# Kernel optimization log

Measured on AMD Instinct MI355X. Metric: run time of the kernel, lower is better.

Reference implementation:

```python
import jax, jax.numpy as jnp
import numpy as np

N_USERS = 100000
N_ITEMS = 50000
N_NODES = N_USERS + N_ITEMS
EMB_DIM = 64
N_EDGES = 1200000
N_LAYERS = 3


def setup_inputs() -> dict:
    key = jax.random.key(0)
    k1, k2, k3, k4, k5 = jax.random.split(key, 5)
    edge_row = jax.random.randint(k1, (N_EDGES,), 0, N_NODES, dtype=jnp.int32)
    edge_col = jax.random.randint(k2, (N_EDGES,), 0, N_NODES, dtype=jnp.int32)
    edge_weight = jax.random.uniform(k3, (N_EDGES,), dtype=jnp.float32)
    # xavier_uniform for nn.Embedding: bound = sqrt(6/(fan_in+fan_out))
    bu = float(np.sqrt(6.0 / (N_USERS + EMB_DIM)))
    bi = float(np.sqrt(6.0 / (N_ITEMS + EMB_DIM)))
    user_emb = jax.random.uniform(k4, (N_USERS, EMB_DIM), jnp.float32, -bu, bu)
    item_emb = jax.random.uniform(k5, (N_ITEMS, EMB_DIM), jnp.float32, -bi, bi)
    return {
        "edge_row": edge_row,
        "edge_col": edge_col,
        "edge_weight": edge_weight,
        "user_emb": user_emb,
        "item_emb": item_emb,
    }


def _spmm(edge_row, edge_col, edge_weight, x):
    # y[i] = sum_{e: row[e]==i} w[e] * x[col[e]]  (COO sparse @ dense)
    gathered = x[edge_col] * edge_weight[:, None]  # [E, d]
    return jax.ops.segment_sum(gathered, edge_row, num_segments=N_NODES)


def reference(edge_row, edge_col, edge_weight, user_emb, item_emb):
    x = jnp.concatenate([user_emb, item_emb], axis=0)  # [N, d]
    acc = x  # running sum over layer outputs (layer 0 = initial embeddings)
    for _ in range(N_LAYERS):
        x = _spmm(edge_row, edge_col, edge_weight, x)
        acc = acc + x
    mean_emb = acc / (N_LAYERS + 1)
    return mean_emb[:N_USERS], mean_emb[N_USERS:]
```

## Files before the change

### kernel.cpp

```cpp
#include <hip/hip_runtime.h>
#include <hip/hip_bf16.h>


#define EMB 64
#define BUCKET_SHIFT 9
#define BROWS (1 << BUCKET_SHIFT)
#define NBUCK_PAD 320
#define S1_CHUNK 2048
#define BCAP 4608
#define S2_CAP 6
#define SPMM_BLOCKS 2048

typedef _Float16 h8 __attribute__((ext_vector_type(8)));
typedef _Float16 h2v __attribute__((ext_vector_type(2)));
typedef float f2v __attribute__((ext_vector_type(2)));
typedef float f4 __attribute__((ext_vector_type(4)));
typedef int i2v __attribute__((ext_vector_type(2)));

union H8U { h8 v; h2v p[4]; };

__global__ void s1_convert(const int* __restrict__ row, const int* __restrict__ col,
                           const float* __restrict__ w, int* __restrict__ cursor1,
                           int2* __restrict__ tmp,
                           const float* __restrict__ ue, const float* __restrict__ ie,
                           h8* __restrict__ X0h, int nu_elems, int total8,
                           int E, int s1Blocks) {
    int t = threadIdx.x;
    if ((int)blockIdx.x < s1Blocks) {
        __shared__ int lcount[NBUCK_PAD];
        __shared__ int lbase[NBUCK_PAD];
        int c0 = blockIdx.x * S1_CHUNK;
        if (t < NBUCK_PAD) lcount[t] = 0;
        __syncthreads();
        int pkc[S1_CHUNK / 512];
        int cc[S1_CHUNK / 512];
        int rr[S1_CHUNK / 512];
        float ww[S1_CHUNK / 512];
        #pragma unroll
        for (int i = 0; i < S1_CHUNK / 512; i++) {
            int e = c0 + i * 512 + t;
            pkc[i] = -1;
            if (e < E) {
                int r = row[e];
                int b = r >> BUCKET_SHIFT;
                int rank = atomicAdd(&lcount[b], 1);
                pkc[i] = (b << 12) | rank;
                cc[i] = col[e];
                rr[i] = r & (BROWS - 1);
                ww[i] = w[e];
            }
        }
        __syncthreads();
        if (t < NBUCK_PAD) {
            int c = lcount[t];
            if (c) lbase[t] = atomicAdd(&cursor1[t], c);
        }
        __syncthreads();
        #pragma unroll
        for (int i = 0; i < S1_CHUNK / 512; i++) {
            if (pkc[i] >= 0) {
                int b = pkc[i] >> 12;
                int pos = lbase[b] + (pkc[i] & 4095);
                if (pos < BCAP)
                    tmp[(size_t)b * BCAP + pos] =
                        make_int2((cc[i] << BUCKET_SHIFT) | rr[i], __float_as_int(ww[i]));
            }
        }
    } else {
        int g = (blockIdx.x - s1Blocks) * 512 + t;
        if (g >= total8) return;
        int base = g << 3;
        const f4* src = (const f4*)((base < nu_elems) ? (ue + base)
                                                      : (ie + (base - nu_elems)));
        f4 a = src[0], b = src[1];
        h8 o;
        o[0] = (_Float16)a.x; o[1] = (_Float16)a.y; o[2] = (_Float16)a.z; o[3] = (_Float16)a.w;
        o[4] = (_Float16)b.x; o[5] = (_Float16)b.y; o[6] = (_Float16)b.z; o[7] = (_Float16)b.w;
        X0h[g] = o;
    }
}

__global__ void scatter2(const int* __restrict__ cursor1, const int2* __restrict__ tmp,
                         int2* __restrict__ cw, int* __restrict__ rbeg,
                         int* __restrict__ rend, int nrows) {
    __shared__ int cnt[BROWS];
    __shared__ int wS[8];
    int t = threadIdx.x;
    int j = blockIdx.x;
    int rowbase = j << BUCKET_SHIFT;
    int rows_here = nrows - rowbase;
    if (rows_here > BROWS) rows_here = BROWS;
    int num = cursor1[j];
    if (num > BCAP) num = BCAP;
    int base = j * BCAP;
    int iters = (num + 1023) >> 10;

    if (t < BROWS) cnt[t] = 0;
    __syncthreads();

    int pkc[S2_CAP];
    int rk[S2_CAP];
    int wv[S2_CAP];
    bool cached = (iters <= S2_CAP);
    if (cached) {
        for (int i = 0; i < iters; i++) {
            int p = i * 1024 + t;
            pkc[i] = -1;
            if (p < num) {
                int2 rec = tmp[base + p];
                pkc[i] = rec.x;
                wv[i] = rec.y;
                rk[i] = atomicAdd(&cnt[rec.x & (BROWS - 1)], 1);
            }
        }
    } else {
        for (int p = t; p < num; p += 1024)
            atomicAdd(&cnt[tmp[base + p].x & (BROWS - 1)], 1);
    }
    __syncthreads();

    int lane = t & 63;
    int wave = t >> 6;
    int v = 0, s = 0;
    if (t < BROWS) {
        v = cnt[t];
        s = v;
        #pragma unroll
        for (int off = 1; off < 64; off <<= 1) {
            int tt = __shfl_up(s, off, 64);
            if (lane >= off) s += tt;
        }
        if (lane == 63) wS[wave] = s;
    }
    __syncthreads();
    if (t < BROWS) {
        int woff = 0;
        for (int w = 0; w < wave; w++) woff += wS[w];
        int excl = woff + s - v;
        if (t < rows_here) {
            rbeg[rowbase + t] = base + excl;
            rend[rowbase + t] = base + excl + v;
        }
        s = excl;
    }
    __syncthreads();
    if (t < BROWS) cnt[t] = s;
    __syncthreads();

    if (cached) {
        for (int i = 0; i < iters; i++) {
            if (pkc[i] >= 0) {
                int r = pkc[i] & (BROWS - 1);
                cw[base + cnt[r] + rk[i]] = make_int2(pkc[i] >> BUCKET_SHIFT, wv[i]);
            }
        }
    } else {
        for (int p = t; p < num; p += 1024) {
            int2 rec = tmp[base + p];
            int r = rec.x & (BROWS - 1);
            int pos = atomicAdd(&cnt[r], 1);
            cw[base + pos] = make_int2(rec.x >> BUCKET_SHIFT, rec.y);
        }
    }
}

template <bool LAST>
__global__ __launch_bounds__(256) void spmm_kernel(
        const int* __restrict__ rbeg, const int* __restrict__ rend,
        const i2v* __restrict__ cw,
        const h8* __restrict__ Xin, h8* __restrict__ Xout,
        const h8* __restrict__ X0, const h8* __restrict__ X1,
        float* __restrict__ out, int nrows) {
    int lane = threadIdx.x & 63;
    int g = lane >> 3;
    int l8 = lane & 7;
    int wv = (blockIdx.x * blockDim.x + threadIdx.x) >> 6;
    int totWaves = (gridDim.x * blockDim.x) >> 6;

    for (int base8 = wv * 8; base8 < nrows; base8 += totWaves * 8) {
        int row = base8 + g;
        bool valid = row < nrows;
        int beg = valid ? rbeg[row] : 0;
        int end = valid ? rend[row] : 0;

        f2v acc2[4];
        #pragma unroll
        for (int k = 0; k < 4; k++) acc2[k] = (f2v){0.f, 0.f};

        int e = beg;
        for (; e + 3 < end; e += 4) {
            i2v c0 = cw[e];
            i2v c1 = cw[e + 1];
            i2v c2 = cw[e + 2];
            i2v c3 = cw[e + 3];
            H8U v0, v1, v2, v3;
            v0.v = Xin[(c0.x << 3) + l8];
            v1.v = Xin[(c1.x << 3) + l8];
            v2.v = Xin[(c2.x << 3) + l8];
            v3.v = Xin[(c3.x << 3) + l8];
            f2v w0p = (f2v){__int_as_float(c0.y), __int_as_float(c0.y)};
            f2v w1p = (f2v){__int_as_float(c1.y), __int_as_float(c1.y)};
            f2v w2p = (f2v){__int_as_float(c2.y), __int_as_float(c2.y)};
            f2v w3p = (f2v){__int_as_float(c3.y), __int_as_float(c3.y)};
            #pragma unroll
            for (int k = 0; k < 4; k++) {
                acc2[k] += w0p * __builtin_convertvector(v0.p[k], f2v);
                acc2[k] += w1p * __builtin_convertvector(v1.p[k], f2v);
                acc2[k] += w2p * __builtin_convertvector(v2.p[k], f2v);
                acc2[k] += w3p * __builtin_convertvector(v3.p[k], f2v);
            }
        }
        for (; e + 1 < end; e += 2) {
            i2v c0 = cw[e];
            i2v c1 = cw[e + 1];
            H8U v0, v1;
            v0.v = Xin[(c0.x << 3) + l8];
            v1.v = Xin[(c1.x << 3) + l8];
            f2v w0p = (f2v){__int_as_float(c0.y), __int_as_float(c0.y)};
            f2v w1p = (f2v){__int_as_float(c1.y), __int_as_float(c1.y)};
            #pragma unroll
            for (int k = 0; k < 4; k++) {
                acc2[k] += w0p * __builtin_convertvector(v0.p[k], f2v);
                acc2[k] += w1p * __builtin_convertvector(v1.p[k], f2v);
            }
        }
        if (e < end) {
            i2v c0 = cw[e];
            H8U v0;
            v0.v = Xin[(c0.x << 3) + l8];
            f2v w0p = (f2v){__int_as_float(c0.y), __int_as_float(c0.y)};
            #pragma unroll
            for (int k = 0; k < 4; k++)
                acc2[k] += w0p * __builtin_convertvector(v0.p[k], f2v);
        }

        float* a = (float*)acc2;
        if (valid) {
            if (LAST) {
                h8 x0 = X0[(row << 3) + l8];
                h8 v1 = X1[(row << 3) + l8];
                h8 v2 = Xin[(row << 3) + l8];
                int base = (row << 6) + (l8 << 3);
                f4 o0, o1;
                o0.x = 0.25f * ((float)x0[0] + (float)v1[0] + (float)v2[0] + a[0]);
                o0.y = 0.25f * ((float)x0[1] + (float)v1[1] + (float)v2[1] + a[1]);
                o0.z = 0.25f * ((float)x0[2] + (float)v1[2] + (float)v2[2] + a[2]);
                o0.w = 0.25f * ((float)x0[3] + (float)v1[3] + (float)v2[3] + a[3]);
                o1.x = 0.25f * ((float)x0[4] + (float)v1[4] + (float)v2[4] + a[4]);
                o1.y = 0.25f * ((float)x0[5] + (float)v1[5] + (float)v2[5] + a[5]);
                o1.z = 0.25f * ((float)x0[6] + (float)v1[6] + (float)v2[6] + a[6]);
                o1.w = 0.25f * ((float)x0[7] + (float)v1[7] + (float)v2[7] + a[7]);
                f4* dst = (f4*)(out + base);
                dst[0] = o0;
                dst[1] = o1;
            } else {
                h8 o;
                #pragma unroll
                for (int k = 0; k < 8; k++) o[k] = (_Float16)a[k];
                Xout[(row << 3) + l8] = o;
            }
        }
    }
}

extern "C" void kernel_launch(void* const* d_in, const int* in_sizes, int n_in,
                              void* d_out, int out_size, void* d_ws, size_t ws_size,
                              hipStream_t stream) {
    const int* edge_row = (const int*)d_in[0];
    const int* edge_col = (const int*)d_in[1];
    const float* edge_w = (const float*)d_in[2];
    const float* user_emb = (const float*)d_in[3];
    const float* item_emb = (const float*)d_in[4];

    const int E = in_sizes[0];
    const int nu_elems = in_sizes[3];
    const int ni_elems = in_sizes[4];
    const int total = nu_elems + ni_elems;
    const int N = total / EMB;
    const int NBUCK = (N + BROWS - 1) >> BUCKET_SHIFT;

    size_t off = 0;
    auto carve = [&](size_t bytes) {
        void* p = (char*)d_ws + off;
        off += (bytes + 255) & ~(size_t)255;
        return p;
    };
    h8*    X0h     = (h8*)carve((size_t)total * 2);
    h8*    X1h     = (h8*)carve((size_t)total * 2);
    h8*    X2h     = (h8*)carve((size_t)total * 2);
    int*   rbeg    = (int*)carve((size_t)N * 4);
    int*   rend    = (int*)carve((size_t)N * 4);
    int*   cursor1 = (int*)carve((size_t)NBUCK * 4);
    int2*  tmp     = (int2*)carve((size_t)NBUCK * BCAP * 8);
    int2*  cw      = (int2*)carve((size_t)NBUCK * BCAP * 8);
    (void)ws_size;

    float* out = (float*)d_out;

    const int total8 = total / 8;
    const int s1Blocks = (E + S1_CHUNK - 1) / S1_CHUNK;
    const int convBlocks = (total8 + 511) / 512;

    hipMemsetAsync(cursor1, 0, (size_t)NBUCK * 4, stream);
    s1_convert<<<s1Blocks + convBlocks, 512, 0, stream>>>(
        edge_row, edge_col, edge_w, cursor1, tmp,
        user_emb, item_emb, X0h, nu_elems, total8, E, s1Blocks);
    scatter2<<<NBUCK, 1024, 0, stream>>>(cursor1, tmp, cw, rbeg, rend, N);

    spmm_kernel<false><<<SPMM_BLOCKS, 256, 0, stream>>>(rbeg, rend, (const i2v*)cw,
                                                        X0h, X1h, nullptr, nullptr,
                                                        nullptr, N);
    spmm_kernel<false><<<SPMM_BLOCKS, 256, 0, stream>>>(rbeg, rend, (const i2v*)cw,
                                                        X1h, X2h, nullptr, nullptr,
                                                        nullptr, N);
    spmm_kernel<true><<<SPMM_BLOCKS, 256, 0, stream>>>(rbeg, rend, (const i2v*)cw,
                                                       X2h, nullptr, X0h, X1h,
                                                       out, N);
}
```

Measured before the change: 222.0 us.

## Sort rows by degree within buckets to balance SpMM wave workload

Within each 256-row bucket, scatter2 now groups rows into degree classes (capped at 31) and writes a permuted slot table (pbeg, pend, prow). SpMM processes slots in that order, so the 8 rows sharing a wave have similar edge counts and lanes sit idle less often. Buckets shrink from 512 to 256 rows and the uncached fallback path is removed, leaving capacity tied to BCAP. The extra prow indirection and padded slots add some memory traffic and scattered output writes.

Result: slower. 260.6 us (+17.4%).

```diff
diff --git a/kernel.cpp b/kernel.cpp
--- a/kernel.cpp
+++ b/kernel.cpp
@@ -3,12 +3,12 @@
 
 
 #define EMB 64
-#define BUCKET_SHIFT 9
+#define BUCKET_SHIFT 8
 #define BROWS (1 << BUCKET_SHIFT)
-#define NBUCK_PAD 320
+#define NBUCK_PAD 592
 #define S1_CHUNK 2048
-#define BCAP 4608
-#define S2_CAP 6
+#define BCAP 2432
+#define S2_CAP 3
 #define SPMM_BLOCKS 2048
 
 typedef _Float16 h8 __attribute__((ext_vector_type(8)));
@@ -30,7 +30,7 @@
         __shared__ int lcount[NBUCK_PAD];
         __shared__ int lbase[NBUCK_PAD];
         int c0 = blockIdx.x * S1_CHUNK;
-        if (t < NBUCK_PAD) lcount[t] = 0;
+        for (int i = t; i < NBUCK_PAD; i += 512) lcount[i] = 0;
         __syncthreads();
         int pkc[S1_CHUNK / 512];
         int cc[S1_CHUNK / 512];
@@ -51,9 +51,9 @@
             }
         }
         __syncthreads();
-        if (t < NBUCK_PAD) {
-            int c = lcount[t];
-            if (c) lbase[t] = atomicAdd(&cursor1[t], c);
+        for (int i = t; i < NBUCK_PAD; i += 512) {
+            int c = lcount[i];
+            if (c) lbase[i] = atomicAdd(&cursor1[i], c);
         }
         __syncthreads();
         #pragma unroll
@@ -81,10 +81,13 @@
 }
 
 __global__ void scatter2(const int* __restrict__ cursor1, const int2* __restrict__ tmp,
-                         int2* __restrict__ cw, int* __restrict__ rbeg,
-                         int* __restrict__ rend, int nrows) {
+                         int2* __restrict__ cw, int* __restrict__ pbeg,
+                         int* __restrict__ pend, int* __restrict__ prow,
+                         int nrows) {
     __shared__ int cnt[BROWS];
-    __shared__ int wS[8];
+    __shared__ int wS[4];
+    __shared__ int ccnt[32];
+    __shared__ int cbase[32];
     int t = threadIdx.x;
     int j = blockIdx.x;
     int rowbase = j << BUCKET_SHIFT;
@@ -96,26 +99,21 @@
     int iters = (num + 1023) >> 10;
 
     if (t < BROWS) cnt[t] = 0;
+    if (t >= BROWS && t < BROWS + 32) ccnt[t - BROWS] = 0;
     __syncthreads();
 
     int pkc[S2_CAP];
     int rk[S2_CAP];
     int wv[S2_CAP];
-    bool cached = (iters <= S2_CAP);
-    if (cached) {
-        for (int i = 0; i < iters; i++) {
-            int p = i * 1024 + t;
-            pkc[i] = -1;
-            if (p < num) {
-                int2 rec = tmp[base + p];
-                pkc[i] = rec.x;
-                wv[i] = rec.y;
-                rk[i] = atomicAdd(&cnt[rec.x & (BROWS - 1)], 1);
-            }
-        }
-    } else {
-        for (int p = t; p < num; p += 1024)
-            atomicAdd(&cnt[tmp[base + p].x & (BROWS - 1)], 1);
+    for (int i = 0; i < iters; i++) {
+        int p = i * 1024 + t;
+        pkc[i] = -1;
+        if (p < num) {
+            int2 rec = tmp[base + p];
+            pkc[i] = rec.x;
+            wv[i] = rec.y;
+            rk[i] = atomicAdd(&cnt[rec.x & (BROWS - 1)], 1);
+        }
     }
     __syncthreads();
 
@@ -133,55 +131,74 @@
         if (lane == 63) wS[wave] = s;
     }
     __syncthreads();
-    if (t < BROWS) {
+    int excl = 0;
+    int dclass = 0, crank = 0;
+    if (t < rows_here) {
         int woff = 0;
         for (int w = 0; w < wave; w++) woff += wS[w];
-        int excl = woff + s - v;
-        if (t < rows_here) {
-            rbeg[rowbase + t] = base + excl;
-            rend[rowbase + t] = base + excl + v;
-        }
-        s = excl;
-    }
-    __syncthreads();
-    if (t < BROWS) cnt[t] = s;
-    __syncthreads();
-
-    if (cached) {
-        for (int i = 0; i < iters; i++) {
-            if (pkc[i] >= 0) {
-                int r = pkc[i] & (BROWS - 1);
-                cw[base + cnt[r] + rk[i]] = make_int2(pkc[i] >> BUCKET_SHIFT, wv[i]);
-            }
-        }
-    } else {
-        for (int p = t; p < num; p += 1024) {
-            int2 rec = tmp[base + p];
-            int r = rec.x & (BROWS - 1);
-            int pos = atomicAdd(&cnt[r], 1);
-            cw[base + pos] = make_int2(rec.x >> BUCKET_SHIFT, rec.y);
+        excl = woff + s - v;
+        dclass = v > 31 ? 31 : v;
+        crank = atomicAdd(&ccnt[dclass], 1);
+    } else if (t < BROWS) {
+        int woff = 0;
+        for (int w = 0; w < wave; w++) woff += wS[w];
+        excl = woff + s - v;
+    }
+    __syncthreads();
+    if (t < 32) {
+        int cs = ccnt[t];
+        int ss = cs;
+        #pragma unroll
+        for (int off = 1; off < 32; off <<= 1) {
+            int tt = __shfl_up(ss, off, 64);
+            if (t >= off) ss += tt;
+        }
+        cbase[t] = ss - cs;
+    }
+    __syncthreads();
+    if (t < rows_here) {
+        int slot = rowbase + cbase[dclass] + crank;
+        pbeg[slot] = base + excl;
+        pend[slot] = base + excl + v;
+        prow[slot] = rowbase + t;
+    } else if (t < BROWS) {
+        int slot = rowbase + t;
+        pbeg[slot] = 0;
+        pend[slot] = 0;
+        prow[slot] = -1;
+    }
+    __syncthreads();
+    if (t < BROWS) cnt[t] = excl;
+    __syncthreads();
+
+    for (int i = 0; i < iters; i++) {
+        if (pkc[i] >= 0) {
+            int r = pkc[i] & (BROWS - 1);
+            cw[base + cnt[r] + rk[i]] = make_int2(pkc[i] >> BUCKET_SHIFT, wv[i]);
         }
     }
 }
 
 template <bool LAST>
 __global__ __launch_bounds__(256) void spmm_kernel(
-        const int* __restrict__ rbeg, const int* __restrict__ rend,
-        const i2v* __restrict__ cw,
+        const int* __restrict__ pbeg, const int* __restrict__ pend,
+        const int* __restrict__ prow, const i2v* __restrict__ cw,
         const h8* __restrict__ Xin, h8* __restrict__ Xout,
         const h8* __restrict__ X0, const h8* __restrict__ X1,
-        float* __restrict__ out, int nrows) {
+        float* __restrict__ out, int nslots) {
     int lane = threadIdx.x & 63;
     int g = lane >> 3;
     int l8 = lane & 7;
     int wv = (blockIdx.x * blockDim.x + threadIdx.x) >> 6;
     int totWaves = (gridDim.x * blockDim.x) >> 6;
 
-    for (int base8 = wv * 8; base8 < nrows; base8 += totWaves * 8) {
-        int row = base8 + g;
-        bool valid = row < nrows;
-        int beg = valid ? rbeg[row] : 0;
-        int end = valid ? rend[row] : 0;
+    for (int base8 = wv * 8; base8 < nslots; base8 += totWaves * 8) {
+        int slot = base8 + g;
+        bool inrange = slot < nslots;
+        int row = inrange ? prow[slot] : -1;
+        bool valid = row >= 0;
+        int beg = inrange ? pbeg[slot] : 0;
+        int end = inrange ? pend[slot] : 0;
 
         f2v acc2[4];
         #pragma unroll
@@ -278,6 +295,7 @@
     const int total = nu_elems + ni_elems;
     const int N = total / EMB;
     const int NBUCK = (N + BROWS - 1) >> BUCKET_SHIFT;
+    const int NSLOTS = NBUCK << BUCKET_SHIFT;
 
     size_t off = 0;
     auto carve = [&](size_t bytes) {
@@ -288,8 +306,9 @@
     h8*    X0h     = (h8*)carve((size_t)total * 2);
     h8*    X1h     = (h8*)carve((size_t)total * 2);
     h8*    X2h     = (h8*)carve((size_t)total * 2);
-    int*   rbeg    = (int*)carve((size_t)N * 4);
-    int*   rend    = (int*)carve((size_t)N * 4);
+    int*   pbeg    = (int*)carve((size_t)NSLOTS * 4);
+    int*   pend    = (int*)carve((size_t)NSLOTS * 4);
+    int*   prow    = (int*)carve((size_t)NSLOTS * 4);
     int*   cursor1 = (int*)carve((size_t)NBUCK * 4);
     int2*  tmp     = (int2*)carve((size_t)NBUCK * BCAP * 8);
     int2*  cw      = (int2*)carve((size_t)NBUCK * BCAP * 8);
@@ -305,15 +324,18 @@
     s1_convert<<<s1Blocks + convBlocks, 512, 0, stream>>>(
         edge_row, edge_col, edge_w, cursor1, tmp,
         user_emb, item_emb, X0h, nu_elems, total8, E, s1Blocks);
-    scatter2<<<NBUCK, 1024, 0, stream>>>(cursor1, tmp, cw, rbeg, rend, N);
-
-    spmm_kernel<false><<<SPMM_BLOCKS, 256, 0, stream>>>(rbeg, rend, (const i2v*)cw,
+    scatter2<<<NBUCK, 1024, 0, stream>>>(cursor1, tmp, cw, pbeg, pend, prow, N);
+
+    spmm_kernel<false><<<SPMM_BLOCKS, 256, 0, stream>>>(pbeg, pend, prow,
+                                                        (const i2v*)cw,
                                                         X0h, X1h, nullptr, nullptr,
-                                                        nullptr, N);
-    spmm_kernel<false><<<SPMM_BLOCKS, 256, 0, stream>>>(rbeg, rend, (const i2v*)cw,
+                                                        nullptr, NSLOTS);
+    spmm_kernel<false><<<SPMM_BLOCKS, 256, 0, stream>>>(pbeg, pend, prow,
+                                                        (const i2v*)cw,
                                                         X1h, X2h, nullptr, nullptr,
-                                                        nullptr, N);
-    spmm_kernel<true><<<SPMM_BLOCKS, 256, 0, stream>>>(rbeg, rend, (const i2v*)cw,
+                                                        nullptr, NSLOTS);
+    spmm_kernel<true><<<SPMM_BLOCKS, 256, 0, stream>>>(pbeg, pend, prow,
+                                                       (const i2v*)cw,
                                                        X2h, nullptr, X0h, X1h,
-                                                       out, N);
+                                                       out, NSLOTS);
 }
```

## Stage bucket scatter through shared memory for coalesced global writes

Applied to the files above, without the earlier changes.

The first-pass bucketing kernel now sorts each chunk's edges by bucket in shared memory and writes them to the global bucket array in contiguous runs instead of scattered per-thread stores. The second-pass row sort likewise places records into an LDS staging buffer and then copies them to the CSR array with coalesced writes. It also drops the non-cached fallback path and lowers S2_CAP, so each bucket is assumed to hold at most 5*1024 records, which BCAP=4608 guarantees. The cost is more shared memory per block, which can reduce occupancy, plus extra barriers.

Result: faster. 214.1 us (-3.6%).

```diff
diff --git a/kernel.cpp b/kernel.cpp
--- a/kernel.cpp
+++ b/kernel.cpp
@@ -8,7 +8,7 @@
 #define NBUCK_PAD 320
 #define S1_CHUNK 2048
 #define BCAP 4608
-#define S2_CAP 6
+#define S2_CAP 5
 #define SPMM_BLOCKS 2048
 
 typedef _Float16 h8 __attribute__((ext_vector_type(8)));
@@ -29,7 +29,13 @@
     if ((int)blockIdx.x < s1Blocks) {
         __shared__ int lcount[NBUCK_PAD];
         __shared__ int lbase[NBUCK_PAD];
+        __shared__ int lexcl[NBUCK_PAD];
+        __shared__ int2 staged[S1_CHUNK];
+        __shared__ short sbkt[S1_CHUNK];
+        __shared__ int swS[8];
         int c0 = blockIdx.x * S1_CHUNK;
+        int chunk_valid = E - c0;
+        if (chunk_valid > S1_CHUNK) chunk_valid = S1_CHUNK;
         if (t < NBUCK_PAD) lcount[t] = 0;
         __syncthreads();
         int pkc[S1_CHUNK / 512];
@@ -51,20 +57,39 @@
             }
         }
         __syncthreads();
-        if (t < NBUCK_PAD) {
-            int c = lcount[t];
-            if (c) lbase[t] = atomicAdd(&cursor1[t], c);
+        int lane = t & 63, wave = t >> 6;
+        int v = (t < NBUCK_PAD) ? lcount[t] : 0;
+        if (t < NBUCK_PAD && v) lbase[t] = atomicAdd(&cursor1[t], v);
+        int s = v;
+        #pragma unroll
+        for (int off = 1; off < 64; off <<= 1) {
+            int tt = __shfl_up(s, off, 64);
+            if (lane >= off) s += tt;
+        }
+        if (lane == 63) swS[wave] = s;
+        __syncthreads();
+        {
+            int woff = 0;
+            for (int wv_ = 0; wv_ < wave; wv_++) woff += swS[wv_];
+            if (t < NBUCK_PAD) lexcl[t] = woff + s - v;
         }
         __syncthreads();
         #pragma unroll
         for (int i = 0; i < S1_CHUNK / 512; i++) {
             if (pkc[i] >= 0) {
                 int b = pkc[i] >> 12;
-                int pos = lbase[b] + (pkc[i] & 4095);
-                if (pos < BCAP)
-                    tmp[(size_t)b * BCAP + pos] =
-                        make_int2((cc[i] << BUCKET_SHIFT) | rr[i], __float_as_int(ww[i]));
-            }
+                int si = lexcl[b] + (pkc[i] & 4095);
+                staged[si] = make_int2((cc[i] << BUCKET_SHIFT) | rr[i],
+                                       __float_as_int(ww[i]));
+                sbkt[si] = (short)b;
+            }
+        }
+        __syncthreads();
+        for (int i = t; i < chunk_valid; i += 512) {
+            int b = sbkt[i];
+            int pos = lbase[b] + (i - lexcl[b]);
+            if (pos < BCAP)
+                tmp[(size_t)b * BCAP + pos] = staged[i];
         }
     } else {
         int g = (blockIdx.x - s1Blocks) * 512 + t;
@@ -84,7 +109,8 @@
                          int2* __restrict__ cw, int* __restrict__ rbeg,
                          int* __restrict__ rend, int nrows) {
     __shared__ int cnt[BROWS];
-    __shared__ int wS[8];
+    __shared__ int wS[16];
+    __shared__ int2 staged[BCAP];
     int t = threadIdx.x;
     int j = blockIdx.x;
     int rowbase = j << BUCKET_SHIFT;
@@ -101,21 +127,15 @@
     int pkc[S2_CAP];
     int rk[S2_CAP];
     int wv[S2_CAP];
-    bool cached = (iters <= S2_CAP);
-    if (cached) {
-        for (int i = 0; i < iters; i++) {
-            int p = i * 1024 + t;
-            pkc[i] = -1;
-            if (p < num) {
-                int2 rec = tmp[base + p];
-                pkc[i] = rec.x;
-                wv[i] = rec.y;
-                rk[i] = atomicAdd(&cnt[rec.x & (BROWS - 1)], 1);
-            }
-        }
-    } else {
-        for (int p = t; p < num; p += 1024)
-            atomicAdd(&cnt[tmp[base + p].x & (BROWS - 1)], 1);
+    for (int i = 0; i < iters; i++) {
+        int p = i * 1024 + t;
+        pkc[i] = -1;
+        if (p < num) {
+            int2 rec = tmp[base + p];
+            pkc[i] = rec.x;
+            wv[i] = rec.y;
+            rk[i] = atomicAdd(&cnt[rec.x & (BROWS - 1)], 1);
+        }
     }
     __syncthreads();
 
@@ -133,35 +153,29 @@
         if (lane == 63) wS[wave] = s;
     }
     __syncthreads();
+    int excl = 0;
     if (t < BROWS) {
         int woff = 0;
         for (int w = 0; w < wave; w++) woff += wS[w];
-        int excl = woff + s - v;
+        excl = woff + s - v;
         if (t < rows_here) {
             rbeg[rowbase + t] = base + excl;
             rend[rowbase + t] = base + excl + v;
         }
-        s = excl;
-    }
-    __syncthreads();
-    if (t < BROWS) cnt[t] = s;
-    __syncthreads();
-
-    if (cached) {
-        for (int i = 0; i < iters; i++) {
-            if (pkc[i] >= 0) {
-                int r = pkc[i] & (BROWS - 1);
-                cw[base + cnt[r] + rk[i]] = make_int2(pkc[i] >> BUCKET_SHIFT, wv[i]);
-            }
-        }
-    } else {
-        for (int p = t; p < num; p += 1024) {
-            int2 rec = tmp[base + p];
-            int r = rec.x & (BROWS - 1);
-            int pos = atomicAdd(&cnt[r], 1);
-            cw[base + pos] = make_int2(rec.x >> BUCKET_SHIFT, rec.y);
-        }
-    }
+    }
+    __syncthreads();
+    if (t < BROWS) cnt[t] = excl;
+    __syncthreads();
+
+    for (int i = 0; i < iters; i++) {
+        if (pkc[i] >= 0) {
+            int r = pkc[i] & (BROWS - 1);
+            staged[cnt[r] + rk[i]] = make_int2(pkc[i] >> BUCKET_SHIFT, wv[i]);
+        }
+    }
+    __syncthreads();
+    for (int p = t; p < num; p += 1024)
+        cw[base + p] = staged[p];
 }
 
 template <bool LAST>
```
